# Performance work log

Measured on AMD Instinct MI355X. Metric: run time of the kernel, lower is better.

## Reference

```python
import jax, jax.numpy as jnp
import numpy as np
from jax import lax

B, W, RSS, NLED, LED_F, HID = 8192, 512, 12, 16, 8, 64


def setup_inputs() -> dict:
    key = jax.random.key(0)
    ks = jax.random.split(key, 20)
    s = 0.05
    return {
        "rss_chunk": jax.random.normal(ks[0], (B, W, RSS), jnp.float32),
        "anchor_pos": jax.random.normal(ks[1], (B, 3), jnp.float32),
        "led_feats": jax.random.normal(ks[2], (NLED, LED_F), jnp.float32),
        "led_positions": jax.random.normal(ks[3], (NLED, 3), jnp.float32),
        "freq_mask": jax.random.randint(ks[4], (RSS, NLED), 0, 2, jnp.int32),
        # temporal_conv params (torch Conv1d weight layout [out, in, k])
        "conv1_w": jax.random.normal(ks[5], (32, RSS, 3), jnp.float32) * s,
        "conv1_b": jax.random.normal(ks[6], (32,), jnp.float32) * s,
        "conv2_w": jax.random.normal(ks[7], (64, 32, 3), jnp.float32) * s,
        "conv2_b": jax.random.normal(ks[8], (64,), jnp.float32) * s,
        # projections (torch Linear weight layout [out, in])
        "q_w": jax.random.normal(ks[9], (64, W + 3), jnp.float32) * s,
        "q_b": jax.random.normal(ks[10], (64,), jnp.float32) * s,
        "k_w": jax.random.normal(ks[11], (64, LED_F + 3), jnp.float32) * s,
        "k_b": jax.random.normal(ks[12], (64,), jnp.float32) * s,
        "red_w": jax.random.normal(ks[13], (64, RSS * LED_F), jnp.float32) * s,
        "red_b": jax.random.normal(ks[14], (64,), jnp.float32) * s,
        "fus_w": jax.random.normal(ks[15], (HID, 64 + 64), jnp.float32) * s,
        "fus_b": jax.random.normal(ks[16], (HID,), jnp.float32) * s,
    }


def _conv1d(x, w, b, stride):
    # x: [B, C_in, L], w: [C_out, C_in, k], padding 1
    y = lax.conv_general_dilated(x, w, (stride,), [(1, 1)],
                                 dimension_numbers=("NCH", "OIH", "NCH"))
    return y + b[None, :, None]


def reference(rss_chunk, anchor_pos, led_feats, led_positions, freq_mask,
              conv1_w, conv1_b, conv2_w, conv2_b,
              q_w, q_b, k_w, k_b, red_w, red_b, fus_w, fus_b):
    Bc = rss_chunk.shape[0]
    x = jnp.swapaxes(rss_chunk, 1, 2)                       # [B, 12, W]

    # temporal conv branch -> [B, 64]
    h = jax.nn.relu(_conv1d(x, conv1_w, conv1_b, 1))        # [B, 32, W]
    h = jax.nn.relu(_conv1d(h, conv2_w, conv2_b, 2))        # [B, 64, W//2]
    t_feat = h.mean(axis=-1)                                # AdaptiveAvgPool1d(1)

    # queries: [B, 12, W+3] -> [B, 12, 64]
    pos_rep = jnp.broadcast_to(anchor_pos[:, None, :], (Bc, RSS, 3))
    query_in = jnp.concatenate([x, pos_rep], axis=-1)
    queries = query_in @ q_w.T + q_b

    # keys: [N, 11] -> [N, 64] (shared across batch)
    key_in = jnp.concatenate([led_feats, led_positions], axis=-1)
    keys = key_in @ k_w.T + k_b

    scores = jnp.einsum("brd,nd->brn", queries, keys)       # [B, 12, N]
    dist_sq = jnp.sum((anchor_pos[:, None, :] - led_positions[None, :, :]) ** 2, -1)
    dist_bias = 0.5 * jnp.log(1.0 / (dist_sq + 1e-8))       # [B, N]
    scores = scores + dist_bias[:, None, :]
    scores = jnp.where(freq_mask[None] == 0, jnp.finfo(scores.dtype).min, scores)

    attn = jax.nn.softmax(scores, axis=-1)                  # [B, 12, N]
    s_agg = jnp.einsum("brn,nf->brf", attn, led_feats)      # [B, 12, 8]
    s_feat = jax.nn.relu(s_agg.reshape(Bc, -1) @ red_w.T + red_b)  # [B, 64]

    combined = jnp.concatenate([t_feat, s_feat], axis=-1)   # [B, 128]
    return combined @ fus_w.T + fus_b                       # [B, hidden]
```

## Files before the change

### kernel.cpp

```cpp
#include <hip/hip_runtime.h>
#include <float.h>
#include <math.h>

typedef __bf16 bf16;
typedef __attribute__((ext_vector_type(8))) __bf16 bf16x8;
typedef __attribute__((ext_vector_type(4))) __bf16 bf16x4;
typedef __attribute__((ext_vector_type(4))) float f32x4;
typedef long long i64;

#define MK 544

#define WS_MG   0
#define WS_CVEC 17408
#define WS_W1F  17472
#define WS_W2F  21568

__device__ __forceinline__ f32x4 mfma16(bf16x8 a, bf16x8 b, f32x4 c) {
  return __builtin_amdgcn_mfma_f32_16x16x32_bf16(a, b, c, 0, 0, 0);
}
__device__ __forceinline__ f32x4 mfma8(i64 a, i64 b, f32x4 c) {
  return __builtin_amdgcn_mfma_f32_16x16x32_fp8_fp8(a, b, c, 0, 0, 0);
}

__global__ __launch_bounds__(256) void acek_pre(
    const float* __restrict__ led_feats, const float* __restrict__ led_pos,
    const float* __restrict__ q_w, const float* __restrict__ q_b,
    const float* __restrict__ k_w, const float* __restrict__ k_b,
    const float* __restrict__ c1w, const float* __restrict__ c2w,
    char* __restrict__ ws) {
  bf16* Mg = (bf16*)(ws + WS_MG);
  float* cvec = (float*)(ws + WS_CVEC);
  bf16x8* W1F = (bf16x8*)(ws + WS_W1F);
  i64* W2F = (i64*)(ws + WS_W2F);
  const int t = threadIdx.x;

  if (blockIdx.x == 34) {
    {
      int ot = t >> 7, s = (t >> 6) & 1, lane = t & 63;
      int g = lane >> 4, a15 = lane & 15;
      bf16x8 f;
#pragma unroll
      for (int j = 0; j < 8; ++j) {
        int k1 = s * 32 + g * 8 + j;
        int dk = k1 >> 4, ic = k1 & 15;
        float v = (ic < 12 && dk < 3) ? c1w[(ot * 16 + a15) * 36 + ic * 3 + dk] : 0.f;
        f[j] = (bf16)v;
      }
      W1F[t] = f;
    }
    for (int r = 0; r < 3; ++r) {
      int fi = t + r * 256;
      int o = fi / 192, rem = fi - o * 192;
      int s = rem >> 6, lane = rem & 63;
      int g = lane >> 4, a15 = lane & 15;
      float v[8];
#pragma unroll
      for (int j = 0; j < 8; ++j)
        v[j] = 16.f * c2w[(o * 16 + a15) * 96 + (g * 8 + j) * 3 + s];
      int lo = __builtin_amdgcn_cvt_pk_fp8_f32(v[0], v[1], 0, false);
      lo = __builtin_amdgcn_cvt_pk_fp8_f32(v[2], v[3], lo, true);
      int hi = __builtin_amdgcn_cvt_pk_fp8_f32(v[4], v[5], 0, false);
      hi = __builtin_amdgcn_cvt_pk_fp8_f32(v[6], v[7], hi, true);
      W2F[fi] = ((i64)(unsigned)lo) | (((i64)hi) << 32);
    }
    return;
  }

  __shared__ float keys[16 * 64];
  for (int idx = t; idx < 16 * 64; idx += 256) {
    int n = idx >> 6, d = idx & 63;
    float acc = k_b[d];
#pragma unroll
    for (int j = 0; j < 8; ++j) acc += k_w[d * 11 + j] * led_feats[n * 8 + j];
#pragma unroll
    for (int j = 0; j < 3; ++j) acc += k_w[d * 11 + 8 + j] * led_pos[n * 3 + j];
    keys[idx] = acc;
  }
  __syncthreads();
  int e = blockIdx.x * 256 + t;
  if (e < 16 * MK) {
    int n = e / MK, k = e - n * MK;
    float v = 0.f;
    if (k < 515) {
#pragma unroll 4
      for (int d = 0; d < 64; ++d) v += q_w[d * 515 + k] * keys[n * 64 + d];
    }
    Mg[e] = (bf16)v;
  }
  if (blockIdx.x == 0 && t < 16) {
    float acc = 0.f;
    for (int d = 0; d < 64; ++d) acc += q_b[d] * keys[t * 64 + d];
    cvec[t] = acc;
  }
}

__global__ __launch_bounds__(256, 4) void acek_main(
    const float* __restrict__ rss, const float* __restrict__ anchor,
    const float* __restrict__ ledf, const float* __restrict__ ledp,
    const int* __restrict__ fmask,
    const float* __restrict__ c1b, const float* __restrict__ c2b,
    const float* __restrict__ rw, const float* __restrict__ rb,
    const float* __restrict__ fw, const float* __restrict__ fb,
    const bf16* __restrict__ Mg, const float* __restrict__ cvec,
    const bf16x8* __restrict__ W1F, const i64* __restrict__ W2F,
    float* __restrict__ out) {

  __shared__ __align__(16) bf16 xw[515 * 16];
  __shared__ __align__(16) unsigned char h1[513 * 40];
  __shared__ __align__(16) float att[192];
  __shared__ __align__(16) float sagg[96];
  __shared__ __align__(16) float comb[128];
  __shared__ __align__(16) float tfp[256];

  const int tid = threadIdx.x;
  const int lane = tid & 63;
  const int wv = tid >> 6;
  const int a15 = lane & 15;
  const int g = lane >> 4;
  const int b = blockIdx.x;
  char* xwb = (char*)xw;
  char* h1b = (char*)h1;

  bf16x8 w1f[2][2];
#pragma unroll
  for (int ot = 0; ot < 2; ++ot)
#pragma unroll
    for (int s = 0; s < 2; ++s) w1f[ot][s] = W1F[(ot * 2 + s) * 64 + lane];
  i64 w2f[4][3];
#pragma unroll
  for (int o = 0; o < 4; ++o)
#pragma unroll
    for (int s = 0; s < 3; ++s) w2f[o][s] = W2F[(o * 3 + s) * 64 + lane];
  f32x4 b1v[2], b2s[4];
#pragma unroll
  for (int ot = 0; ot < 2; ++ot) b1v[ot] = *(const f32x4*)&c1b[ot * 16 + g * 4];
#pragma unroll
  for (int o = 0; o < 4; ++o) {
    f32x4 tmp = *(const f32x4*)&c2b[o * 16 + g * 4];
    b2s[o] = tmp * 16.f;
  }

  bf16x4 z4 = {(bf16)0.f, (bf16)0.f, (bf16)0.f, (bf16)0.f};
  for (int r = tid; r < 515; r += 256)
    *(bf16x4*)(xwb + r * 32 + (24 ^ ((r & 4) << 2))) = z4;
  if (tid < 12) {
    int rr = (tid >> 2) == 0 ? 0 : ((tid >> 2) == 1 ? 513 : 514);
    *(bf16x4*)(xwb + rr * 32 + (((tid & 3) * 8) ^ ((rr & 4) << 2))) = z4;
  }
  if (tid < 4) *(i64*)(h1b + tid * 8) = 0;

  const float* xb = rss + (size_t)b * 6144;
#pragma unroll
  for (int i = 0; i < 6; ++i) {
    int f = tid + i * 256;
    f32x4 v = ((const f32x4*)xb)[f];
    int w = f / 3;
    int c = (f - w * 3) * 4;
    bf16x4 bv;
    bv[0] = (bf16)v[0]; bv[1] = (bf16)v[1]; bv[2] = (bf16)v[2]; bv[3] = (bf16)v[3];
    int row = w + 1;
    *(bf16x4*)(xwb + row * 32 + ((c * 2) ^ ((row & 4) << 2))) = bv;
  }
  __syncthreads();

  auto conv1_tile = [&](int wt) {
    const int dk0 = g >> 1;
    const int icb16 = (g & 1) << 4;
    const int wcol = wt * 16 + a15;
    f32x4 c0 = {0.f, 0.f, 0.f, 0.f}, c1 = {0.f, 0.f, 0.f, 0.f};
#pragma unroll
    for (int s = 0; s < 2; ++s) {
      int row = wcol + 2 * s + dk0;
      bf16x8 bv = *(const bf16x8*)(xwb + row * 32 + (icb16 ^ ((row & 4) << 2)));
      c0 = mfma16(w1f[0][s], bv, c0);
      c1 = mfma16(w1f[1][s], bv, c1);
    }
    const int hrow = wcol + 1;
    float v0 = fmaxf(c0[0] + b1v[0][0], 0.f), v1 = fmaxf(c0[1] + b1v[0][1], 0.f);
    float v2 = fmaxf(c0[2] + b1v[0][2], 0.f), v3 = fmaxf(c0[3] + b1v[0][3], 0.f);
    int pk0 = __builtin_amdgcn_cvt_pk_fp8_f32(v0, v1, 0, false);
    pk0 = __builtin_amdgcn_cvt_pk_fp8_f32(v2, v3, pk0, true);
    *(int*)(h1b + hrow * 40 + g * 4) = pk0;
    v0 = fmaxf(c1[0] + b1v[1][0], 0.f); v1 = fmaxf(c1[1] + b1v[1][1], 0.f);
    v2 = fmaxf(c1[2] + b1v[1][2], 0.f); v3 = fmaxf(c1[3] + b1v[1][3], 0.f);
    int pk1 = __builtin_amdgcn_cvt_pk_fp8_f32(v0, v1, 0, false);
    pk1 = __builtin_amdgcn_cvt_pk_fp8_f32(v2, v3, pk1, true);
    *(int*)(h1b + hrow * 40 + 16 + g * 4) = pk1;
  };

  if (wv < 3) {
    const int base = wv * 10;
#pragma unroll
    for (int t = 0; t < 10; ++t) conv1_tile(base + t);
  } else {
    conv1_tile(30);
    conv1_tile(31);
    const float anc0 = anchor[(size_t)b * 3 + 0];
    const float anc1 = anchor[(size_t)b * 3 + 1];
    const float anc2 = anchor[(size_t)b * 3 + 2];
    const bf16* MgR = Mg + a15 * MK;
    f32x4 sac = {0.f, 0.f, 0.f, 0.f};
#pragma unroll
    for (int s = 0; s < 16; ++s) {
      bf16x8 av;
#pragma unroll
      for (int j = 0; j < 8; ++j) {
        int row = s * 32 + g * 8 + j + 1;
        av[j] = *(const bf16*)(xwb + row * 32 + ((a15 * 2) ^ ((row & 4) << 2)));
      }
      bf16x8 bm = *(const bf16x8*)&MgR[s * 32 + g * 8];
      sac = mfma16(av, bm, sac);
    }
    {
      bf16x8 av = {(bf16)0.f, (bf16)0.f, (bf16)0.f, (bf16)0.f,
                   (bf16)0.f, (bf16)0.f, (bf16)0.f, (bf16)0.f};
      if (g == 0) { av[0] = (bf16)anc0; av[1] = (bf16)anc1; av[2] = (bf16)anc2; }
      bf16x8 bm = *(const bf16x8*)&MgR[512 + g * 8];
      sac = mfma16(av, bm, sac);
    }
    float dx = anc0 - ledp[a15 * 3 + 0];
    float dy = anc1 - ledp[a15 * 3 + 1];
    float dz = anc2 - ledp[a15 * 3 + 2];
    float cv = cvec[a15] - 0.5f * __logf(dx * dx + dy * dy + dz * dz + 1e-8f);
#pragma unroll
    for (int rho = 0; rho < 4; ++rho) {
      int r = 4 * g + rho;
      int mrow = (r < 12) ? r : 11;
      float sc = sac[rho] + cv;
      if (fmask[mrow * 16 + a15] == 0) sc = -FLT_MAX;
      float mx = sc;
      mx = fmaxf(mx, __shfl_xor(mx, 1, 16));
      mx = fmaxf(mx, __shfl_xor(mx, 2, 16));
      mx = fmaxf(mx, __shfl_xor(mx, 4, 16));
      mx = fmaxf(mx, __shfl_xor(mx, 8, 16));
      float ev = __expf(sc - mx);
      float sm = ev;
      sm += __shfl_xor(sm, 1, 16);
      sm += __shfl_xor(sm, 2, 16);
      sm += __shfl_xor(sm, 4, 16);
      sm += __shfl_xor(sm, 8, 16);
      if (r < 12) att[r * 16 + a15] = ev / sm;
    }
    for (int it = lane; it < 96; it += 64) {
      int r = it >> 3, f = it & 7;
      float acc = 0.f;
#pragma unroll
      for (int n = 0; n < 16; ++n) acc += att[r * 16 + n] * ledf[n * 8 + f];
      sagg[it] = acc;
    }
  }
  __syncthreads();

  {
    float tacc[4][4] = {{0.f, 0.f, 0.f, 0.f}, {0.f, 0.f, 0.f, 0.f},
                        {0.f, 0.f, 0.f, 0.f}, {0.f, 0.f, 0.f, 0.f}};
#pragma unroll
    for (int pti = 0; pti < 4; ++pti) {
      const int p = (wv * 4 + pti) * 16 + a15;
      f32x4 cc0 = {0.f, 0.f, 0.f, 0.f}, cc1 = {0.f, 0.f, 0.f, 0.f};
      f32x4 cc2 = {0.f, 0.f, 0.f, 0.f}, cc3 = {0.f, 0.f, 0.f, 0.f};
#pragma unroll
      for (int s = 0; s < 3; ++s) {
        i64 hv = *(const i64*)(h1b + (2 * p + s) * 40 + g * 8);
        cc0 = mfma8(w2f[0][s], hv, cc0);
        cc1 = mfma8(w2f[1][s], hv, cc1);
        cc2 = mfma8(w2f[2][s], hv, cc2);
        cc3 = mfma8(w2f[3][s], hv, cc3);
      }
#pragma unroll
      for (int r = 0; r < 4; ++r) {
        tacc[0][r] += fmaxf(cc0[r] + b2s[0][r], 0.f);
        tacc[1][r] += fmaxf(cc1[r] + b2s[1][r], 0.f);
        tacc[2][r] += fmaxf(cc2[r] + b2s[2][r], 0.f);
        tacc[3][r] += fmaxf(cc3[r] + b2s[3][r], 0.f);
      }
    }
#pragma unroll
    for (int o = 0; o < 4; ++o)
#pragma unroll
      for (int r = 0; r < 4; ++r) {
        float v = tacc[o][r];
        v += __shfl_xor(v, 1, 16);
        v += __shfl_xor(v, 2, 16);
        v += __shfl_xor(v, 4, 16);
        v += __shfl_xor(v, 8, 16);
        if (a15 == 0) tfp[wv * 64 + o * 16 + g * 4 + r] = v;
      }
  }
  __syncthreads();

  if (tid < 64)
    comb[tid] = (tfp[tid] + tfp[64 + tid] + tfp[128 + tid] + tfp[192 + tid]) *
                (1.f / 4096.f);
  {
    const int o = tid >> 2, q = tid & 3;
    float acc = 0.f;
    const f32x4* rwv = (const f32x4*)(rw + o * 96 + q * 24);
    const f32x4* sv = (const f32x4*)(sagg + q * 24);
#pragma unroll
    for (int i = 0; i < 6; ++i) {
      f32x4 a = rwv[i], s = sv[i];
      acc += a[0] * s[0] + a[1] * s[1] + a[2] * s[2] + a[3] * s[3];
    }
    acc += __shfl_xor(acc, 1, 4);
    acc += __shfl_xor(acc, 2, 4);
    if (q == 0) comb[64 + o] = fmaxf(acc + rb[o], 0.f);
  }
  __syncthreads();

  {
    const int o = tid >> 2, q = tid & 3;
    float acc = 0.f;
    const f32x4* fwv = (const f32x4*)(fw + o * 128 + q * 32);
    const f32x4* cv = (const f32x4*)(comb + q * 32);
#pragma unroll
    for (int i = 0; i < 8; ++i) {
      f32x4 a = fwv[i], c = cv[i];
      acc += a[0] * c[0] + a[1] * c[1] + a[2] * c[2] + a[3] * c[3];
    }
    acc += __shfl_xor(acc, 1, 4);
    acc += __shfl_xor(acc, 2, 4);
    if (q == 0) out[(size_t)b * 64 + o] = acc + fb[o];
  }
}

extern "C" void kernel_launch(void* const* d_in, const int* in_sizes, int n_in,
                              void* d_out, int out_size, void* d_ws, size_t ws_size,
                              hipStream_t stream) {
  (void)in_sizes; (void)n_in; (void)out_size; (void)ws_size;
  const float* rss   = (const float*)d_in[0];
  const float* anch  = (const float*)d_in[1];
  const float* ledf  = (const float*)d_in[2];
  const float* ledp  = (const float*)d_in[3];
  const int*   fmask = (const int*)d_in[4];
  const float* c1w = (const float*)d_in[5];
  const float* c1b = (const float*)d_in[6];
  const float* c2w = (const float*)d_in[7];
  const float* c2b = (const float*)d_in[8];
  const float* qw  = (const float*)d_in[9];
  const float* qb  = (const float*)d_in[10];
  const float* kw  = (const float*)d_in[11];
  const float* kb  = (const float*)d_in[12];
  const float* rw  = (const float*)d_in[13];
  const float* rb  = (const float*)d_in[14];
  const float* fw  = (const float*)d_in[15];
  const float* fb  = (const float*)d_in[16];
  float* outp = (float*)d_out;
  char* ws = (char*)d_ws;

  acek_pre<<<35, 256, 0, stream>>>(ledf, ledp, qw, qb, kw, kb, c1w, c2w, ws);
  acek_main<<<8192, 256, 0, stream>>>(
      rss, anch, ledf, ledp, fmask, c1b, c2b, rw, rb, fw, fb,
      (const bf16*)(ws + WS_MG), (const float*)(ws + WS_CVEC),
      (const bf16x8*)(ws + WS_W1F), (const i64*)(ws + WS_W2F), outp);
}
```

Measured before the change: 147.2 us.

## Run conv1 in fp8 with compact LDS, swizzled h1, and raise occupancy

Conv1 now uses FP8 MFMA: the input window is stored in LDS as scaled fp8 (16 bytes per row instead of 32) and the conv1 weights are prepacked as fp8, with the scale undone in the epilogue. The h1 buffer shrinks to a 32-byte stride with an XOR swizzle, and the scratch buffers tfp/comb alias the input window. Together these shrink LDS use so launch bounds can rise to 6 blocks per CU. The query path now reads rss straight from global memory in bf16 instead of from LDS, and conv1 tiles are rebalanced across three waves. Reducing conv1 precision to fp8 risks accuracy, and the strided global reads in the attention wave may cost latency.

```diff
diff --git a/kernel.cpp b/kernel.cpp
--- a/kernel.cpp
+++ b/kernel.cpp
@@ -4,7 +4,6 @@
 
 typedef __bf16 bf16;
 typedef __attribute__((ext_vector_type(8))) __bf16 bf16x8;
-typedef __attribute__((ext_vector_type(4))) __bf16 bf16x4;
 typedef __attribute__((ext_vector_type(4))) float f32x4;
 typedef long long i64;
 
@@ -13,7 +12,7 @@
 #define WS_MG   0
 #define WS_CVEC 17408
 #define WS_W1F  17472
-#define WS_W2F  21568
+#define WS_W2F  19520
 
 __device__ __forceinline__ f32x4 mfma16(bf16x8 a, bf16x8 b, f32x4 c) {
   return __builtin_amdgcn_mfma_f32_16x16x32_bf16(a, b, c, 0, 0, 0);
@@ -30,7 +29,7 @@
     char* __restrict__ ws) {
   bf16* Mg = (bf16*)(ws + WS_MG);
   float* cvec = (float*)(ws + WS_CVEC);
-  bf16x8* W1F = (bf16x8*)(ws + WS_W1F);
+  i64* W1F = (i64*)(ws + WS_W1F);
   i64* W2F = (i64*)(ws + WS_W2F);
   const int t = threadIdx.x;
 
@@ -38,15 +37,18 @@
     {
       int ot = t >> 7, s = (t >> 6) & 1, lane = t & 63;
       int g = lane >> 4, a15 = lane & 15;
-      bf16x8 f;
+      float v[8];
 #pragma unroll
       for (int j = 0; j < 8; ++j) {
         int k1 = s * 32 + g * 8 + j;
         int dk = k1 >> 4, ic = k1 & 15;
-        float v = (ic < 12 && dk < 3) ? c1w[(ot * 16 + a15) * 36 + ic * 3 + dk] : 0.f;
-        f[j] = (bf16)v;
+        v[j] = (ic < 12 && dk < 3) ? 16.f * c1w[(ot * 16 + a15) * 36 + ic * 3 + dk] : 0.f;
       }
-      W1F[t] = f;
+      int lo = __builtin_amdgcn_cvt_pk_fp8_f32(v[0], v[1], 0, false);
+      lo = __builtin_amdgcn_cvt_pk_fp8_f32(v[2], v[3], lo, true);
+      int hi = __builtin_amdgcn_cvt_pk_fp8_f32(v[4], v[5], 0, false);
+      hi = __builtin_amdgcn_cvt_pk_fp8_f32(v[6], v[7], hi, true);
+      W1F[t] = ((i64)(unsigned)lo) | (((i64)hi) << 32);
     }
     for (int r = 0; r < 3; ++r) {
       int fi = t + r * 256;
@@ -94,7 +96,7 @@
   }
 }
 
-__global__ __launch_bounds__(256, 4) void acek_main(
+__global__ __launch_bounds__(256, 6) void acek_main(
     const float* __restrict__ rss, const float* __restrict__ anchor,
     const float* __restrict__ ledf, const float* __restrict__ ledp,
     const int* __restrict__ fmask,
@@ -102,15 +104,15 @@
     const float* __restrict__ rw, const float* __restrict__ rb,
     const float* __restrict__ fw, const float* __restrict__ fb,
     const bf16* __restrict__ Mg, const float* __restrict__ cvec,
-    const bf16x8* __restrict__ W1F, const i64* __restrict__ W2F,
+    const i64* __restrict__ W1F, const i64* __restrict__ W2F,
     float* __restrict__ out) {
 
-  __shared__ __align__(16) bf16 xw[515 * 16];
-  __shared__ __align__(16) unsigned char h1[513 * 40];
+  __shared__ __align__(16) unsigned char xw8[515 * 16];
+  __shared__ __align__(16) unsigned char h1[513 * 32];
   __shared__ __align__(16) float att[192];
   __shared__ __align__(16) float sagg[96];
-  __shared__ __align__(16) float comb[128];
-  __shared__ __align__(16) float tfp[256];
+  float* tfp = (float*)xw8;
+  float* comb = (float*)(xw8 + 4096);
 
   const int tid = threadIdx.x;
   const int lane = tid & 63;
@@ -118,10 +120,10 @@
   const int a15 = lane & 15;
   const int g = lane >> 4;
   const int b = blockIdx.x;
-  char* xwb = (char*)xw;
+  char* xwb = (char*)xw8;
   char* h1b = (char*)h1;
 
-  bf16x8 w1f[2][2];
+  i64 w1f[2][2];
 #pragma unroll
   for (int ot = 0; ot < 2; ++ot)
 #pragma unroll
@@ -140,12 +142,10 @@
     b2s[o] = tmp * 16.f;
   }
 
-  bf16x4 z4 = {(bf16)0.f, (bf16)0.f, (bf16)0.f, (bf16)0.f};
-  for (int r = tid; r < 515; r += 256)
-    *(bf16x4*)(xwb + r * 32 + (24 ^ ((r & 4) << 2))) = z4;
+  for (int r = tid; r < 515; r += 256) *(int*)(xwb + r * 16 + 12) = 0;
   if (tid < 12) {
     int rr = (tid >> 2) == 0 ? 0 : ((tid >> 2) == 1 ? 513 : 514);
-    *(bf16x4*)(xwb + rr * 32 + (((tid & 3) * 8) ^ ((rr & 4) << 2))) = z4;
+    *(int*)(xwb + rr * 16 + (tid & 3) * 4) = 0;
   }
   if (tid < 4) *(i64*)(h1b + tid * 8) = 0;
 
@@ -156,58 +156,59 @@
     f32x4 v = ((const f32x4*)xb)[f];
     int w = f / 3;
     int c = (f - w * 3) * 4;
-    bf16x4 bv;
-    bv[0] = (bf16)v[0]; bv[1] = (bf16)v[1]; bv[2] = (bf16)v[2]; bv[3] = (bf16)v[3];
-    int row = w + 1;
-    *(bf16x4*)(xwb + row * 32 + ((c * 2) ^ ((row & 4) << 2))) = bv;
+    int pk = __builtin_amdgcn_cvt_pk_fp8_f32(16.f * v[0], 16.f * v[1], 0, false);
+    pk = __builtin_amdgcn_cvt_pk_fp8_f32(16.f * v[2], 16.f * v[3], pk, true);
+    *(int*)(xwb + (w + 1) * 16 + c) = pk;
   }
   __syncthreads();
 
   auto conv1_tile = [&](int wt) {
-    const int dk0 = g >> 1;
-    const int icb16 = (g & 1) << 4;
     const int wcol = wt * 16 + a15;
     f32x4 c0 = {0.f, 0.f, 0.f, 0.f}, c1 = {0.f, 0.f, 0.f, 0.f};
 #pragma unroll
     for (int s = 0; s < 2; ++s) {
-      int row = wcol + 2 * s + dk0;
-      bf16x8 bv = *(const bf16x8*)(xwb + row * 32 + (icb16 ^ ((row & 4) << 2)));
-      c0 = mfma16(w1f[0][s], bv, c0);
-      c1 = mfma16(w1f[1][s], bv, c1);
+      int row = wcol + 2 * s + (g >> 1);
+      i64 bv = *(const i64*)(xwb + row * 16 + ((g & 1) << 3));
+      c0 = mfma8(w1f[0][s], bv, c0);
+      c1 = mfma8(w1f[1][s], bv, c1);
     }
     const int hrow = wcol + 1;
-    float v0 = fmaxf(c0[0] + b1v[0][0], 0.f), v1 = fmaxf(c0[1] + b1v[0][1], 0.f);
-    float v2 = fmaxf(c0[2] + b1v[0][2], 0.f), v3 = fmaxf(c0[3] + b1v[0][3], 0.f);
+    const int swz = (hrow >> 2) & 3;
+    const int off0 = ((((g >> 1) + 0) ^ swz) << 3) | ((g & 1) << 2);
+    const int off1 = ((((g >> 1) + 2) ^ swz) << 3) | ((g & 1) << 2);
+    float v0 = fmaxf(fmaf(c0[0], 0.00390625f, b1v[0][0]), 0.f);
+    float v1 = fmaxf(fmaf(c0[1], 0.00390625f, b1v[0][1]), 0.f);
+    float v2 = fmaxf(fmaf(c0[2], 0.00390625f, b1v[0][2]), 0.f);
+    float v3 = fmaxf(fmaf(c0[3], 0.00390625f, b1v[0][3]), 0.f);
     int pk0 = __builtin_amdgcn_cvt_pk_fp8_f32(v0, v1, 0, false);
     pk0 = __builtin_amdgcn_cvt_pk_fp8_f32(v2, v3, pk0, true);
-    *(int*)(h1b + hrow * 40 + g * 4) = pk0;
-    v0 = fmaxf(c1[0] + b1v[1][0], 0.f); v1 = fmaxf(c1[1] + b1v[1][1], 0.f);
-    v2 = fmaxf(c1[2] + b1v[1][2], 0.f); v3 = fmaxf(c1[3] + b1v[1][3], 0.f);
+    *(int*)(h1b + hrow * 32 + off0) = pk0;
+    v0 = fmaxf(fmaf(c1[0], 0.00390625f, b1v[1][0]), 0.f);
+    v1 = fmaxf(fmaf(c1[1], 0.00390625f, b1v[1][1]), 0.f);
+    v2 = fmaxf(fmaf(c1[2], 0.00390625f, b1v[1][2]), 0.f);
+    v3 = fmaxf(fmaf(c1[3], 0.00390625f, b1v[1][3]), 0.f);
     int pk1 = __builtin_amdgcn_cvt_pk_fp8_f32(v0, v1, 0, false);
     pk1 = __builtin_amdgcn_cvt_pk_fp8_f32(v2, v3, pk1, true);
-    *(int*)(h1b + hrow * 40 + 16 + g * 4) = pk1;
+    *(int*)(h1b + hrow * 32 + off1) = pk1;
   };
 
   if (wv < 3) {
-    const int base = wv * 10;
-#pragma unroll
-    for (int t = 0; t < 10; ++t) conv1_tile(base + t);
+    const int base = wv * 11;
+    const int n = (wv == 2) ? 10 : 11;
+    for (int t = 0; t < n; ++t) conv1_tile(base + t);
   } else {
-    conv1_tile(30);
-    conv1_tile(31);
     const float anc0 = anchor[(size_t)b * 3 + 0];
     const float anc1 = anchor[(size_t)b * 3 + 1];
     const float anc2 = anchor[(size_t)b * 3 + 2];
+    const int rcl = (a15 < 12) ? a15 : 11;
     const bf16* MgR = Mg + a15 * MK;
     f32x4 sac = {0.f, 0.f, 0.f, 0.f};
-#pragma unroll
+#pragma unroll 4
     for (int s = 0; s < 16; ++s) {
+      const float* xs = xb + (s * 32 + g * 8) * 12 + rcl;
       bf16x8 av;
 #pragma unroll
-      for (int j = 0; j < 8; ++j) {
-        int row = s * 32 + g * 8 + j + 1;
-        av[j] = *(const bf16*)(xwb + row * 32 + ((a15 * 2) ^ ((row & 4) << 2)));
-      }
+      for (int j = 0; j < 8; ++j) av[j] = (bf16)xs[j * 12];
       bf16x8 bm = *(const bf16x8*)&MgR[s * 32 + g * 8];
       sac = mfma16(av, bm, sac);
     }
@@ -261,7 +262,8 @@
       f32x4 cc2 = {0.f, 0.f, 0.f, 0.f}, cc3 = {0.f, 0.f, 0.f, 0.f};
 #pragma unroll
       for (int s = 0; s < 3; ++s) {
-        i64 hv = *(const i64*)(h1b + (2 * p + s) * 40 + g * 8);
+        const int rho = 2 * p + s;
+        i64 hv = *(const i64*)(h1b + rho * 32 + ((g ^ ((rho >> 2) & 3)) << 3));
         cc0 = mfma8(w2f[0][s], hv, cc0);
         cc1 = mfma8(w2f[1][s], hv, cc1);
         cc2 = mfma8(w2f[2][s], hv, cc2);
@@ -352,5 +354,5 @@
   acek_main<<<8192, 256, 0, stream>>>(
       rss, anch, ledf, ledp, fmask, c1b, c2b, rw, rb, fw, fb,
       (const bf16*)(ws + WS_MG), (const float*)(ws + WS_CVEC),
-      (const bf16x8*)(ws + WS_W1F), (const i64*)(ws + WS_W2F), outp);
-}
+      (const i64*)(ws + WS_W1F), (const i64*)(ws + WS_W2F), outp);
+}
```

Result: slower. 265.2 us (+80.2%).
